# Optimization experiments

Measured on AMD Instinct MI355X. Metric: run time of the kernel, lower is better.

The kernel has to match this reference:

```python
import jax, jax.numpy as jnp
import numpy as np

N = 100000
DIM = 32
E = 1600000
K = 1.0      # stiffness
L0 = 0.1     # rest length


def setup_inputs() -> dict:
    key = jax.random.key(0)
    k1, k2 = jax.random.split(key)
    # Points on the Lorentz hyperboloid: x0 = sqrt(1 + |x_spatial|^2)
    spatial = 0.5 * jax.random.normal(k1, (N, DIM - 1), dtype=jnp.float32)
    x0 = jnp.sqrt(1.0 + jnp.sum(spatial * spatial, axis=-1, keepdims=True))
    x = jnp.concatenate([x0, spatial], axis=-1)  # (N, DIM)
    edges = jax.random.randint(k2, (E, 2), 0, N, dtype=jnp.int64)
    return {"x": x, "edges": edges}


def reference(x, edges):
    u_idx = edges[:, 0]
    v_idx = edges[:, 1]
    xu = x[u_idx]                                  # (E, DIM) gather
    xv = x[v_idx]                                  # (E, DIM) gather
    J = jnp.ones((x.shape[-1],), dtype=x.dtype).at[0].set(-1.0)  # Minkowski metric sign
    inner = jnp.sum(xu * xv * J, axis=-1)          # (E,) Lorentz inner product
    inner = jnp.minimum(inner, -1.0 - 1e-7)        # clamp(max=-1-1e-7)
    dist = jnp.arccosh(-inner)                     # hyperbolic distance
    delta = dist - L0
    total_energy = jnp.sum(0.5 * K * delta * delta)
    denom = jnp.sqrt(inner * inner - 1.0)
    factor = -(K * delta / (denom + 1e-9))[:, None]  # (E,1)
    grad = jnp.zeros_like(x)
    grad = grad.at[u_idx].add(factor * (xv * J))   # scatter-add
    grad = grad.at[v_idx].add(factor * (xu * J))
    return total_energy, grad
```

## Files before the change

### kernel.cpp

```cpp
#include <hip/hip_runtime.h>
#include <hip/hip_fp16.h>
#include <math.h>

#define DIM      32
#define HDIM     16
#define N_NODES  100000
#define N_EDGES  1600000
#define L0       0.1f

__global__ __launch_bounds__(256) void spring_edge_f16_kernel(
    const float*  __restrict__ x,
    const int*    __restrict__ edges,
    __half2*      __restrict__ grad_h,
    float*        __restrict__ energy_ws)
{
    const int tid   = threadIdx.x;
    const int lane  = tid & 63;
    const int k     = lane & 15;
    const int quad  = lane >> 4;
    const int qId   = ((blockIdx.x * blockDim.x + tid) >> 6) * 4 + quad;
    const int nQuad = ((gridDim.x * blockDim.x) >> 6) * 4;

    const float2* __restrict__ x2 = (const float2*)x;
    const float Jx = (k == 0) ? -1.0f : 1.0f;

    double energy = 0.0;

    for (int e0 = qId; e0 < N_EDGES; e0 += 2 * nQuad) {
        const int  e1 = e0 + nQuad;
        const bool a1 = (e1 < N_EDGES);

        const int2 ev0 = ((const int2*)edges)[e0];
        const int2 ev1 = a1 ? ((const int2*)edges)[e1] : make_int2(0, 0);
        const float2 xu0 = x2[ev0.x * HDIM + k];
        const float2 xv0 = x2[ev0.y * HDIM + k];
        const float2 xu1 = x2[ev1.x * HDIM + k];
        const float2 xv1 = x2[ev1.y * HDIM + k];

        float p0 = Jx * xu0.x * xv0.x + xu0.y * xv0.y;
        float p1 = Jx * xu1.x * xv1.x + xu1.y * xv1.y;
        #pragma unroll
        for (int off = 8; off; off >>= 1) {
            p0 += __shfl_xor(p0, off, 16);
            p1 += __shfl_xor(p1, off, 16);
        }

        {
            const float inner = fminf(p0, -1.0000001f);
            const float zm1   = -inner - 1.0f;
            const float s     = sqrtf(zm1 * (zm1 + 2.0f));
            const float dist  = log1pf(zm1 + s);
            const float delta = dist - L0;
            const float f     = -delta / (s + 1e-9f);
            unsafeAtomicAdd(&grad_h[ev0.x * HDIM + k],
                            __floats2half2_rn(f * Jx * xv0.x, f * xv0.y));
            unsafeAtomicAdd(&grad_h[ev0.y * HDIM + k],
                            __floats2half2_rn(f * Jx * xu0.x, f * xu0.y));
            if (k == 0) energy += 0.5 * (double)delta * (double)delta;
        }
        if (a1) {
            const float inner = fminf(p1, -1.0000001f);
            const float zm1   = -inner - 1.0f;
            const float s     = sqrtf(zm1 * (zm1 + 2.0f));
            const float dist  = log1pf(zm1 + s);
            const float delta = dist - L0;
            const float f     = -delta / (s + 1e-9f);
            unsafeAtomicAdd(&grad_h[ev1.x * HDIM + k],
                            __floats2half2_rn(f * Jx * xv1.x, f * xv1.y));
            unsafeAtomicAdd(&grad_h[ev1.y * HDIM + k],
                            __floats2half2_rn(f * Jx * xu1.x, f * xu1.y));
            if (k == 0) energy += 0.5 * (double)delta * (double)delta;
        }
    }

    #pragma unroll
    for (int off = 32; off; off >>= 1)
        energy += __shfl_xor(energy, off, 64);

    __shared__ double s_e[4];
    if (lane == 0) s_e[tid >> 6] = energy;
    __syncthreads();
    if (tid == 0)
        atomicAdd(energy_ws, (float)(s_e[0] + s_e[1] + s_e[2] + s_e[3]));
}

__global__ __launch_bounds__(256) void convert_kernel(
    const __half2* __restrict__ grad_h,
    const float*   __restrict__ energy_ws,
    float*         __restrict__ out)
{
    const int i = blockIdx.x * 256 + threadIdx.x;
    if (i < N_NODES * HDIM) {
        const float2 f = __half22float2(grad_h[i]);
        out[1 + 2 * i]     = f.x;
        out[1 + 2 * i + 1] = f.y;
    }
    if (i == 0) out[0] = *energy_ws;
}

__global__ __launch_bounds__(256) void spring_edge_kernel(
    const float* __restrict__ x,
    const int*   __restrict__ edges,
    float*       __restrict__ out)
{
    const int tid    = threadIdx.x;
    const int lane   = tid & 63;
    const int d      = lane & 31;
    const int half   = lane >> 5;
    const int waveId = (blockIdx.x * blockDim.x + tid) >> 6;
    const int nWaves = (gridDim.x * blockDim.x) >> 6;

    float* __restrict__ grad = out + 1;
    const float Jd = (d == 0) ? -1.0f : 1.0f;
    double energy = 0.0;

    for (int e0 = waveId * 2; e0 < N_EDGES; e0 += nWaves * 2) {
        const int  e      = e0 + half;
        const bool active = (e < N_EDGES);
        int u = 0, v = 0;
        float xu = 0.0f, xv = 0.0f;
        if (active) {
            u  = edges[2 * e];
            v  = edges[2 * e + 1];
            xu = x[u * DIM + d];
            xv = x[v * DIM + d];
        }
        float p = xu * xv;
        if (d == 0) p = -p;
        #pragma unroll
        for (int off = 16; off; off >>= 1)
            p += __shfl_xor(p, off, 32);

        const float inner  = fminf(p, -1.0000001f);
        const float zm1    = -inner - 1.0f;
        const float s      = sqrtf(zm1 * (zm1 + 2.0f));
        const float dist   = log1pf(zm1 + s);
        const float delta  = dist - L0;
        const float factor = -delta / (s + 1e-9f);

        if (active) {
            atomicAdd(&grad[u * DIM + d], factor * xv * Jd);
            atomicAdd(&grad[v * DIM + d], factor * xu * Jd);
            if (d == 0)
                energy += 0.5 * (double)delta * (double)delta;
        }
    }
    #pragma unroll
    for (int off = 32; off; off >>= 1)
        energy += __shfl_xor(energy, off, 64);
    __shared__ double s_e[4];
    if (lane == 0) s_e[tid >> 6] = energy;
    __syncthreads();
    if (tid == 0)
        atomicAdd(&out[0], (float)(s_e[0] + s_e[1] + s_e[2] + s_e[3]));
}

extern "C" void kernel_launch(void* const* d_in, const int* in_sizes, int n_in,
                              void* d_out, int out_size, void* d_ws, size_t ws_size,
                              hipStream_t stream) {
    const float* x     = (const float*)d_in[0];
    const int*   edges = (const int*)d_in[1];
    float*       out   = (float*)d_out;

    const size_t grad_bytes = (size_t)N_NODES * HDIM * sizeof(__half2);
    const size_t need       = grad_bytes + sizeof(float);

    if (ws_size >= need) {
        __half2* grad_h    = (__half2*)d_ws;
        float*   energy_ws = (float*)((char*)d_ws + grad_bytes);

        hipMemsetAsync(d_ws, 0, need, stream);
        spring_edge_f16_kernel<<<4096, 256, 0, stream>>>(x, edges, grad_h,
                                                         energy_ws);
        convert_kernel<<<(N_NODES * HDIM + 255) / 256, 256, 0, stream>>>(
            grad_h, energy_ws, out);
    } else {
        hipMemsetAsync(out, 0, (size_t)out_size * sizeof(float), stream);
        spring_edge_kernel<<<4096, 256, 0, stream>>>(x, edges, out);
    }
}
```

Measured before the change: 266.3 us.

## Replace atomic scatter-add with per-call CSR build and gather-based gradient accumulation

Adds a path that builds a node-to-edge CSR adjacency on each call (histogram, multi-kernel prefix scan, then a fill pass that computes per-edge force factors and energy). A gather kernel then accumulates each node's gradient in registers and writes it once in full fp32. This removes the fp16 packed atomic scatter-adds and the convert kernel. In exchange it adds several launches, per-edge atomics on the cursor array, a 25.6MB adjacency buffer and a second random gather of x. It runs only when the workspace is large enough.

```diff
diff --git a/kernel.cpp b/kernel.cpp
--- a/kernel.cpp
+++ b/kernel.cpp
@@ -7,6 +7,204 @@
 #define N_NODES  100000
 #define N_EDGES  1600000
 #define L0       0.1f
+#define NB_SCAN  ((N_NODES + 255) / 256)
+
+
+__global__ __launch_bounds__(256) void hist_kernel(
+    const int* __restrict__ edges, int* __restrict__ counts)
+{
+    const int i      = blockIdx.x * blockDim.x + threadIdx.x;
+    const int stride = gridDim.x * blockDim.x;
+    for (int e = i; e < N_EDGES; e += stride) {
+        const int2 ev = ((const int2*)edges)[e];
+        atomicAdd(&counts[ev.x], 1);
+        atomicAdd(&counts[ev.y], 1);
+    }
+}
+
+__global__ __launch_bounds__(256) void reduce_counts_kernel(
+    const int* __restrict__ counts, int* __restrict__ blockSums)
+{
+    __shared__ int s[256];
+    const int t = threadIdx.x;
+    const int i = blockIdx.x * 256 + t;
+    s[t] = (i < N_NODES) ? counts[i] : 0;
+    __syncthreads();
+    #pragma unroll
+    for (int off = 128; off; off >>= 1) {
+        if (t < off) s[t] += s[t + off];
+        __syncthreads();
+    }
+    if (t == 0) blockSums[blockIdx.x] = s[0];
+}
+
+__global__ __launch_bounds__(512) void scan_sums_kernel(int* __restrict__ blockSums)
+{
+    __shared__ int s[512];
+    const int t = threadIdx.x;
+    const int v = (t < NB_SCAN) ? blockSums[t] : 0;
+    s[t] = v;
+    __syncthreads();
+    for (int off = 1; off < 512; off <<= 1) {
+        const int add = (t >= off) ? s[t - off] : 0;
+        __syncthreads();
+        s[t] += add;
+        __syncthreads();
+    }
+    if (t < NB_SCAN) blockSums[t] = s[t] - v;
+}
+
+__global__ __launch_bounds__(256) void scan_counts_kernel(
+    int* __restrict__ counts, const int* __restrict__ blockSums)
+{
+    __shared__ int s[256];
+    const int t = threadIdx.x;
+    const int i = blockIdx.x * 256 + t;
+    const int v = (i < N_NODES) ? counts[i] : 0;
+    s[t] = v;
+    __syncthreads();
+    for (int off = 1; off < 256; off <<= 1) {
+        const int add = (t >= off) ? s[t - off] : 0;
+        __syncthreads();
+        s[t] += add;
+        __syncthreads();
+    }
+    if (i < N_NODES) counts[i] = s[t] - v + blockSums[blockIdx.x];
+}
+
+__global__ __launch_bounds__(256) void csr_fill_kernel(
+    const float* __restrict__ x,
+    const int*   __restrict__ edges,
+    int*         __restrict__ cursor,
+    int2*        __restrict__ adj,
+    float*       __restrict__ out)
+{
+    const int tid   = threadIdx.x;
+    const int lane  = tid & 63;
+    const int k     = lane & 15;
+    const int quad  = lane >> 4;
+    const int qId   = ((blockIdx.x * blockDim.x + tid) >> 6) * 4 + quad;
+    const int nQuad = ((gridDim.x * blockDim.x) >> 6) * 4;
+
+    const float2* __restrict__ x2 = (const float2*)x;
+    const float Jx = (k == 0) ? -1.0f : 1.0f;
+
+    double energy = 0.0;
+
+    for (int e0 = qId; e0 < N_EDGES; e0 += 2 * nQuad) {
+        const int  e1 = e0 + nQuad;
+        const bool a1 = (e1 < N_EDGES);
+
+        const int2 ev0 = ((const int2*)edges)[e0];
+        const int2 ev1 = a1 ? ((const int2*)edges)[e1] : make_int2(0, 0);
+
+        int pu0 = 0, pv0 = 0, pu1 = 0, pv1 = 0;
+        if (k == 0) {
+            pu0 = atomicAdd(&cursor[ev0.x], 1);
+            pv0 = atomicAdd(&cursor[ev0.y], 1);
+            if (a1) {
+                pu1 = atomicAdd(&cursor[ev1.x], 1);
+                pv1 = atomicAdd(&cursor[ev1.y], 1);
+            }
+        }
+
+        const float2 xu0 = x2[ev0.x * HDIM + k];
+        const float2 xv0 = x2[ev0.y * HDIM + k];
+        const float2 xu1 = x2[ev1.x * HDIM + k];
+        const float2 xv1 = x2[ev1.y * HDIM + k];
+
+        float p0 = Jx * xu0.x * xv0.x + xu0.y * xv0.y;
+        float p1 = Jx * xu1.x * xv1.x + xu1.y * xv1.y;
+        #pragma unroll
+        for (int off = 8; off; off >>= 1) {
+            p0 += __shfl_xor(p0, off, 16);
+            p1 += __shfl_xor(p1, off, 16);
+        }
+
+        {
+            const float inner = fminf(p0, -1.0000001f);
+            const float zm1   = -inner - 1.0f;
+            const float s     = sqrtf(zm1 * (zm1 + 2.0f));
+            const float dist  = log1pf(zm1 + s);
+            const float delta = dist - L0;
+            const float f     = -delta / (s + 1e-9f);
+            if (k == 0) {
+                adj[pu0] = make_int2(ev0.y, __float_as_int(f));
+                adj[pv0] = make_int2(ev0.x, __float_as_int(f));
+                energy += 0.5 * (double)delta * (double)delta;
+            }
+        }
+        if (a1) {
+            const float inner = fminf(p1, -1.0000001f);
+            const float zm1   = -inner - 1.0f;
+            const float s     = sqrtf(zm1 * (zm1 + 2.0f));
+            const float dist  = log1pf(zm1 + s);
+            const float delta = dist - L0;
+            const float f     = -delta / (s + 1e-9f);
+            if (k == 0) {
+                adj[pu1] = make_int2(ev1.y, __float_as_int(f));
+                adj[pv1] = make_int2(ev1.x, __float_as_int(f));
+                energy += 0.5 * (double)delta * (double)delta;
+            }
+        }
+    }
+
+    #pragma unroll
+    for (int off = 32; off; off >>= 1)
+        energy += __shfl_xor(energy, off, 64);
+    __shared__ double s_e[4];
+    if (lane == 0) s_e[tid >> 6] = energy;
+    __syncthreads();
+    if (tid == 0)
+        atomicAdd(out, (float)(s_e[0] + s_e[1] + s_e[2] + s_e[3]));
+}
+
+__global__ __launch_bounds__(256) void csr_gather_kernel(
+    const float* __restrict__ x,
+    const int*   __restrict__ ends,
+    const int2*  __restrict__ adj,
+    float*       __restrict__ out)
+{
+    const int tid   = threadIdx.x;
+    const int lane  = tid & 63;
+    const int k     = lane & 15;
+    const int quad  = lane >> 4;
+    const int qId   = ((blockIdx.x * blockDim.x + tid) >> 6) * 4 + quad;
+    const int nQuad = ((gridDim.x * blockDim.x) >> 6) * 4;
+
+    const float2* __restrict__ x2 = (const float2*)x;
+    const float Jx = (k == 0) ? -1.0f : 1.0f;
+    float* __restrict__ grad = out + 1;
+
+    for (int n = qId; n < N_NODES; n += nQuad) {
+        const int start = (n == 0) ? 0 : ends[n - 1];
+        const int end   = ends[n];
+
+        float accx = 0.0f, accy = 0.0f;
+        int i = start;
+        for (; i + 1 < end; i += 2) {
+            const int2  a0  = adj[i];
+            const int2  a1  = adj[i + 1];
+            const float2 x0 = x2[a0.x * HDIM + k];
+            const float2 x1 = x2[a1.x * HDIM + k];
+            const float f0  = __int_as_float(a0.y);
+            const float f1  = __int_as_float(a1.y);
+            accx = fmaf(f0, Jx * x0.x, accx);
+            accy = fmaf(f0, x0.y, accy);
+            accx = fmaf(f1, Jx * x1.x, accx);
+            accy = fmaf(f1, x1.y, accy);
+        }
+        if (i < end) {
+            const int2  a0  = adj[i];
+            const float2 x0 = x2[a0.x * HDIM + k];
+            const float f0  = __int_as_float(a0.y);
+            accx = fmaf(f0, Jx * x0.x, accx);
+            accy = fmaf(f0, x0.y, accy);
+        }
+        grad[n * DIM + 2 * k]     = accx;
+        grad[n * DIM + 2 * k + 1] = accy;
+    }
+}
 
 __global__ __launch_bounds__(256) void spring_edge_f16_kernel(
     const float*  __restrict__ x,
@@ -162,14 +360,34 @@
     const int*   edges = (const int*)d_in[1];
     float*       out   = (float*)d_out;
 
+    const size_t counts_bytes = (size_t)N_NODES * sizeof(int);
+    const size_t bsums_off    = (counts_bytes + 255) & ~(size_t)255;
+    const size_t bsums_bytes  = (size_t)NB_SCAN * sizeof(int);
+    const size_t adj_off      = (bsums_off + bsums_bytes + 255) & ~(size_t)255;
+    const size_t adj_bytes    = (size_t)2 * N_EDGES * sizeof(int2);
+    const size_t csr_need     = adj_off + adj_bytes;
+
     const size_t grad_bytes = (size_t)N_NODES * HDIM * sizeof(__half2);
-    const size_t need       = grad_bytes + sizeof(float);
-
-    if (ws_size >= need) {
+    const size_t f16_need   = grad_bytes + sizeof(float);
+
+    if (ws_size >= csr_need) {
+        int*  counts = (int*)d_ws;
+        int*  bsums  = (int*)((char*)d_ws + bsums_off);
+        int2* adj    = (int2*)((char*)d_ws + adj_off);
+
+        hipMemsetAsync(counts, 0, counts_bytes, stream);
+        hipMemsetAsync(out, 0, sizeof(float), stream);
+        hist_kernel<<<2048, 256, 0, stream>>>(edges, counts);
+        reduce_counts_kernel<<<NB_SCAN, 256, 0, stream>>>(counts, bsums);
+        scan_sums_kernel<<<1, 512, 0, stream>>>(bsums);
+        scan_counts_kernel<<<NB_SCAN, 256, 0, stream>>>(counts, bsums);
+        csr_fill_kernel<<<4096, 256, 0, stream>>>(x, edges, counts, adj, out);
+        csr_gather_kernel<<<2048, 256, 0, stream>>>(x, counts, adj, out);
+    } else if (ws_size >= f16_need) {
         __half2* grad_h    = (__half2*)d_ws;
         float*   energy_ws = (float*)((char*)d_ws + grad_bytes);
 
-        hipMemsetAsync(d_ws, 0, need, stream);
+        hipMemsetAsync(d_ws, 0, f16_need, stream);
         spring_edge_f16_kernel<<<4096, 256, 0, stream>>>(x, edges, grad_h,
                                                          energy_ws);
         convert_kernel<<<(N_NODES * HDIM + 255) / 256, 256, 0, stream>>>(
```

After: 450.3 us. +69.1%, slower.

## Bin edge endpoints by destination node block and accumulate gradients in LDS

Applied to the files above, without the earlier changes.

Adds a binning pass that splits each edge into two directed records and scatters them into 256 per-block buckets, each covering 391 nodes. A gather kernel then handles one bucket per workgroup, accumulating gradients in shared memory with fp32 LDS atomics and writing them out once, which replaces global fp16 atomics and the convert pass. This trades global atomic contention for an extra pass over the edges and a fixed per-bucket capacity: records past CAP are silently dropped. Energy is split as 0.25 per directed record.

```diff
diff --git a/kernel.cpp b/kernel.cpp
--- a/kernel.cpp
+++ b/kernel.cpp
@@ -7,6 +7,158 @@
 #define N_NODES  100000
 #define N_EDGES  1600000
 #define L0       0.1f
+
+#define NB       256
+#define NPB      391
+#define CAP      14336
+#define TILE     2048
+#define NT       ((N_EDGES + TILE - 1) / TILE)
+
+
+__global__ __launch_bounds__(256) void bin_kernel(
+    const int*    __restrict__ edges,
+    unsigned int* __restrict__ gcursor,
+    unsigned int* __restrict__ recs_g)
+{
+    __shared__ unsigned int  recs[2 * TILE];
+    __shared__ unsigned int  srec[2 * TILE];
+    __shared__ unsigned char rb  [2 * TILE];
+    __shared__ unsigned char srb [2 * TILE];
+    __shared__ unsigned int  hist [NB];
+    __shared__ unsigned int  lscan[NB];
+    __shared__ unsigned int  gbase[NB];
+    __shared__ unsigned int  cnt  [NB];
+
+    const int t    = threadIdx.x;
+    const int base = blockIdx.x * TILE;
+    const int nedge = min(TILE, N_EDGES - base);
+    const int nrec  = 2 * nedge;
+
+    hist[t] = 0;
+    cnt[t]  = 0;
+    __syncthreads();
+
+    #pragma unroll
+    for (int i = 0; i < TILE / 256; ++i) {
+        const int e = base + i * 256 + t;
+        if (e < N_EDGES) {
+            const int2 ev = ((const int2*)edges)[e];
+            const int bu = ev.x / NPB;
+            const int du = ev.x - bu * NPB;
+            const int bv = ev.y / NPB;
+            const int dv = ev.y - bv * NPB;
+            const int r0 = (i * 256 + t) * 2;
+            recs[r0]     = (unsigned)du | ((unsigned)ev.y << 9);
+            rb[r0]       = (unsigned char)bu;
+            recs[r0 + 1] = (unsigned)dv | ((unsigned)ev.x << 9);
+            rb[r0 + 1]   = (unsigned char)bv;
+            atomicAdd(&hist[bu], 1u);
+            atomicAdd(&hist[bv], 1u);
+        }
+    }
+    __syncthreads();
+
+    lscan[t] = hist[t];
+    __syncthreads();
+    for (int off = 1; off < NB; off <<= 1) {
+        const unsigned add = (t >= off) ? lscan[t - off] : 0u;
+        __syncthreads();
+        lscan[t] += add;
+        __syncthreads();
+    }
+    const unsigned myCnt = hist[t];
+    gbase[t] = myCnt ? atomicAdd(&gcursor[t], myCnt) : 0u;
+    const unsigned excl = lscan[t] - myCnt;
+    __syncthreads();
+    lscan[t] = excl;
+    __syncthreads();
+
+    for (int r = t; r < nrec; r += 256) {
+        const unsigned char b  = rb[r];
+        const unsigned int  lo = atomicAdd(&cnt[b], 1u);
+        const unsigned int  pos = lscan[b] + lo;
+        srec[pos] = recs[r];
+        srb[pos]  = b;
+    }
+    __syncthreads();
+
+    for (int j = t; j < nrec; j += 256) {
+        const unsigned char b   = srb[j];
+        const unsigned int  idx = gbase[b] + ((unsigned)j - lscan[b]);
+        if (idx < CAP)
+            recs_g[(unsigned)b * CAP + idx] = srec[j];
+    }
+}
+
+__global__ __launch_bounds__(1024) void gather_kernel(
+    const float*        __restrict__ x,
+    const unsigned int* __restrict__ recs_g,
+    const unsigned int* __restrict__ gcursor,
+    float*              __restrict__ out)
+{
+    __shared__ float  lg[NPB * DIM];
+    __shared__ double s_e[16];
+
+    const int b     = blockIdx.x;
+    const int t     = threadIdx.x;
+    const int lane  = t & 63;
+    const int k     = lane & 15;
+    const int qId   = (t >> 6) * 4 + (lane >> 4);
+    const int node0 = b * NPB;
+    const int nnode = min(NPB, N_NODES - node0);
+
+    for (int j = t; j < NPB * DIM; j += 1024) lg[j] = 0.0f;
+    __syncthreads();
+
+    const int nrec = min((int)gcursor[b], CAP);
+    const float2* __restrict__ x2 = (const float2*)x;
+    const float Jx = (k == 0) ? -1.0f : 1.0f;
+
+    double energy = 0.0;
+
+    for (int i = qId; i < nrec; i += 64) {
+        const unsigned int rec = recs_g[b * CAP + i];
+        const int dl = (int)(rec & 511u);
+        const int nb = (int)(rec >> 9);
+
+        const float2 xn = x2[nb * HDIM + k];
+        const float2 xd = x2[(node0 + dl) * HDIM + k];
+
+        float p = Jx * xd.x * xn.x + xd.y * xn.y;
+        #pragma unroll
+        for (int off = 8; off; off >>= 1)
+            p += __shfl_xor(p, off, 16);
+
+        const float inner = fminf(p, -1.0000001f);
+        const float zm1   = -inner - 1.0f;
+        const float s     = sqrtf(zm1 * (zm1 + 2.0f));
+        const float dist  = log1pf(zm1 + s);
+        const float delta = dist - L0;
+        const float f     = -delta / (s + 1e-9f);
+
+        atomicAdd(&lg[dl * DIM + 2 * k],     f * Jx * xn.x);
+        atomicAdd(&lg[dl * DIM + 2 * k + 1], f * xn.y);
+        if (k == 0)
+            energy += 0.25 * (double)delta * (double)delta;
+    }
+
+    #pragma unroll
+    for (int off = 32; off; off >>= 1)
+        energy += __shfl_xor(energy, off, 64);
+    if (lane == 0) s_e[t >> 6] = energy;
+    __syncthreads();
+    if (t == 0) {
+        double tot = 0.0;
+        #pragma unroll
+        for (int w = 0; w < 16; ++w) tot += s_e[w];
+        atomicAdd(&out[0], (float)tot);
+    }
+
+    float* __restrict__ grad = out + 1;
+    const int lim = nnode * DIM;
+    for (int j = t; j < lim; j += 1024)
+        grad[node0 * DIM + j] = lg[j];
+}
 
 __global__ __launch_bounds__(256) void spring_edge_f16_kernel(
     const float*  __restrict__ x,
@@ -162,14 +314,27 @@
     const int*   edges = (const int*)d_in[1];
     float*       out   = (float*)d_out;
 
+    const size_t cur_bytes = (size_t)NB * sizeof(unsigned int);
+    const size_t rec_off   = 1024;
+    const size_t rec_bytes = (size_t)NB * CAP * sizeof(unsigned int);
+    const size_t bin_need  = rec_off + rec_bytes;
+
     const size_t grad_bytes = (size_t)N_NODES * HDIM * sizeof(__half2);
-    const size_t need       = grad_bytes + sizeof(float);
-
-    if (ws_size >= need) {
+    const size_t f16_need   = grad_bytes + sizeof(float);
+
+    if (ws_size >= bin_need) {
+        unsigned int* gcursor = (unsigned int*)d_ws;
+        unsigned int* recs_g  = (unsigned int*)((char*)d_ws + rec_off);
+
+        hipMemsetAsync(gcursor, 0, cur_bytes, stream);
+        hipMemsetAsync(out, 0, sizeof(float), stream);
+        bin_kernel<<<NT, 256, 0, stream>>>(edges, gcursor, recs_g);
+        gather_kernel<<<NB, 1024, 0, stream>>>(x, recs_g, gcursor, out);
+    } else if (ws_size >= f16_need) {
         __half2* grad_h    = (__half2*)d_ws;
         float*   energy_ws = (float*)((char*)d_ws + grad_bytes);
 
-        hipMemsetAsync(d_ws, 0, need, stream);
+        hipMemsetAsync(d_ws, 0, f16_need, stream);
         spring_edge_f16_kernel<<<4096, 256, 0, stream>>>(x, edges, grad_h,
                                                          energy_ws);
         convert_kernel<<<(N_NODES * HDIM + 255) / 256, 256, 0, stream>>>(
```

After: 749.1 us. 2.81x slower.

## Fuse memset, edge kernel and convert into one cooperative kernel with grid syncs

Applied to the files above, without the earlier changes.

Replaces the three-launch sequence (memset, edge scatter kernel, half-to-float convert) with a single cooperative kernel of 2048 blocks. It zeroes the workspace, runs the edge pass, and does the conversion, separated by two grid-wide syncs. The aim is to remove launch gaps and per-kernel tail overheads. In exchange it uses half the blocks of the earlier edge kernel, which can reduce latency hiding for the gather and atomics. It also relies on cooperative launch succeeding, with a fallback to the old path if it does not.

```diff
diff --git a/kernel.cpp b/kernel.cpp
--- a/kernel.cpp
+++ b/kernel.cpp
@@ -1,12 +1,123 @@
 #include <hip/hip_runtime.h>
+#include <hip/hip_cooperative_groups.h>
 #include <hip/hip_fp16.h>
 #include <math.h>
+
+namespace cg = cooperative_groups;
 
 #define DIM      32
 #define HDIM     16
 #define N_NODES  100000
 #define N_EDGES  1600000
 #define L0       0.1f
+
+#define COOP_BLOCKS   2048
+#define COOP_THREADS  256
+
+__global__ __launch_bounds__(256, 8) void fused_coop_kernel(
+    const float*  __restrict__ x,
+    const int*    __restrict__ edges,
+    __half2*      __restrict__ grad_h,
+    float*        __restrict__ energy_ws,
+    float*        __restrict__ out)
+{
+    cg::grid_group grid = cg::this_grid();
+
+    const int tid  = threadIdx.x;
+    const int gtid = blockIdx.x * COOP_THREADS + tid;
+    const int nthr = gridDim.x * COOP_THREADS;
+
+    {
+        uint4* g4 = (uint4*)grad_h;
+        const int n4 = N_NODES * HDIM / 4;
+        for (int i = gtid; i < n4; i += nthr)
+            g4[i] = make_uint4(0u, 0u, 0u, 0u);
+        if (gtid == 0) *energy_ws = 0.0f;
+    }
+    grid.sync();
+
+    {
+        const int lane  = tid & 63;
+        const int k     = lane & 15;
+        const int quad  = lane >> 4;
+        const int qId   = ((blockIdx.x * blockDim.x + tid) >> 6) * 4 + quad;
+        const int nQuad = ((gridDim.x * blockDim.x) >> 6) * 4;
+
+        const float2* __restrict__ x2 = (const float2*)x;
+        const float Jx = (k == 0) ? -1.0f : 1.0f;
+
+        double energy = 0.0;
+
+        for (int e0 = qId; e0 < N_EDGES; e0 += 2 * nQuad) {
+            const int  e1 = e0 + nQuad;
+            const bool a1 = (e1 < N_EDGES);
+
+            const int2 ev0 = ((const int2*)edges)[e0];
+            const int2 ev1 = a1 ? ((const int2*)edges)[e1] : make_int2(0, 0);
+            const float2 xu0 = x2[ev0.x * HDIM + k];
+            const float2 xv0 = x2[ev0.y * HDIM + k];
+            const float2 xu1 = x2[ev1.x * HDIM + k];
+            const float2 xv1 = x2[ev1.y * HDIM + k];
+
+            float p0 = Jx * xu0.x * xv0.x + xu0.y * xv0.y;
+            float p1 = Jx * xu1.x * xv1.x + xu1.y * xv1.y;
+            #pragma unroll
+            for (int off = 8; off; off >>= 1) {
+                p0 += __shfl_xor(p0, off, 16);
+                p1 += __shfl_xor(p1, off, 16);
+            }
+
+            {
+                const float inner = fminf(p0, -1.0000001f);
+                const float zm1   = -inner - 1.0f;
+                const float s     = sqrtf(zm1 * (zm1 + 2.0f));
+                const float dist  = log1pf(zm1 + s);
+                const float delta = dist - L0;
+                const float f     = -delta / (s + 1e-9f);
+                unsafeAtomicAdd(&grad_h[ev0.x * HDIM + k],
+                                __floats2half2_rn(f * Jx * xv0.x, f * xv0.y));
+                unsafeAtomicAdd(&grad_h[ev0.y * HDIM + k],
+                                __floats2half2_rn(f * Jx * xu0.x, f * xu0.y));
+                if (k == 0) energy += 0.5 * (double)delta * (double)delta;
+            }
+            if (a1) {
+                const float inner = fminf(p1, -1.0000001f);
+                const float zm1   = -inner - 1.0f;
+                const float s     = sqrtf(zm1 * (zm1 + 2.0f));
+                const float dist  = log1pf(zm1 + s);
+                const float delta = dist - L0;
+                const float f     = -delta / (s + 1e-9f);
+                unsafeAtomicAdd(&grad_h[ev1.x * HDIM + k],
+                                __floats2half2_rn(f * Jx * xv1.x, f * xv1.y));
+                unsafeAtomicAdd(&grad_h[ev1.y * HDIM + k],
+                                __floats2half2_rn(f * Jx * xu1.x, f * xu1.y));
+                if (k == 0) energy += 0.5 * (double)delta * (double)delta;
+            }
+        }
+
+        #pragma unroll
+        for (int off = 32; off; off >>= 1)
+            energy += __shfl_xor(energy, off, 64);
+
+        __shared__ double s_e[4];
+        if (lane == 0) s_e[tid >> 6] = energy;
+        __syncthreads();
+        if (tid == 0)
+            atomicAdd(energy_ws,
+                      (float)(s_e[0] + s_e[1] + s_e[2] + s_e[3]));
+    }
+    grid.sync();
+
+    {
+        const int lim = N_NODES * HDIM;
+        for (int i = gtid; i < lim; i += nthr) {
+            const float2 f = __half22float2(grad_h[i]);
+            out[1 + 2 * i]     = f.x;
+            out[1 + 2 * i + 1] = f.y;
+        }
+        if (gtid == 0) out[0] = *energy_ws;
+    }
+}
 
 __global__ __launch_bounds__(256) void spring_edge_f16_kernel(
     const float*  __restrict__ x,
@@ -169,11 +280,21 @@
         __half2* grad_h    = (__half2*)d_ws;
         float*   energy_ws = (float*)((char*)d_ws + grad_bytes);
 
-        hipMemsetAsync(d_ws, 0, need, stream);
-        spring_edge_f16_kernel<<<4096, 256, 0, stream>>>(x, edges, grad_h,
-                                                         energy_ws);
-        convert_kernel<<<(N_NODES * HDIM + 255) / 256, 256, 0, stream>>>(
-            grad_h, energy_ws, out);
+        void* kargs[] = {
+            (void*)&x, (void*)&edges, (void*)&grad_h,
+            (void*)&energy_ws, (void*)&out
+        };
+        const hipError_t err = hipLaunchCooperativeKernel(
+            (void*)fused_coop_kernel,
+            dim3(COOP_BLOCKS), dim3(COOP_THREADS), kargs, 0, stream);
+
+        if (err != hipSuccess) {
+            hipMemsetAsync(d_ws, 0, need, stream);
+            spring_edge_f16_kernel<<<4096, 256, 0, stream>>>(x, edges, grad_h,
+                                                             energy_ws);
+            convert_kernel<<<(N_NODES * HDIM + 255) / 256, 256, 0, stream>>>(
+                grad_h, energy_ws, out);
+        }
     } else {
         hipMemsetAsync(out, 0, (size_t)out_size * sizeof(float), stream);
         spring_edge_kernel<<<4096, 256, 0, stream>>>(x, edges, out);
```

New measurement: 597.7 us. 124% more time.
